# Kernel optimization log

Hardware: AMD Instinct MI355X
Metric: run time of the kernel (lower is better)

Reference implementation:

```python
import jax, jax.numpy as jnp
import numpy as np

DIMS = [64, 128, 192, 256]   # Matryoshka sub-dims (init arg `dims`)
TEMPERATURE = 1.0
NEG_INF = float('-inf')
EPS = 1e-12  # F.normalize eps


def setup_inputs() -> dict:
    key = jax.random.key(0)
    k1, k2 = jax.random.split(key)
    B, K, D = 2048, 4096, 256
    reps_q = jax.random.normal(k1, (B, D), dtype=jnp.float32)
    reps_d = jax.random.normal(k2, (K, D), dtype=jnp.float32)
    return {"reps_q": reps_q, "reps_d": reps_d}


def _l2_normalize(x):
    n = jnp.linalg.norm(x, axis=1, keepdims=True)
    return x / jnp.maximum(n, EPS)


def _loss_for_dim(reps_q, reps_d, dim):
    q = _l2_normalize(reps_q[:, :dim])   # [B, dim]
    d = _l2_normalize(reps_d[:, :dim])   # [K, dim]
    B, K = q.shape[0], d.shape[0]

    qk = q @ d.T                         # [B, K]

    # check_pos_neg_pair_conflict (always True in the torch code)
    pos = d[:B]                          # positives are the first B keys
    sim = jax.lax.stop_gradient(pos @ d.T)               # [B, K], detached
    eye_bk = jnp.eye(B, K, dtype=bool)
    conflict = jnp.isclose(sim, 1.0, rtol=1e-5, atol=1e-5) & ~eye_bk
    qk = jnp.where(conflict, NEG_INF, qk)

    # use_all_pairs=True path: kq, qq, kk with -inf diagonals
    eye_bb = jnp.eye(B, dtype=bool)
    kq = jnp.where(eye_bb, NEG_INF, pos @ q.T)           # [B, B]
    qq = jnp.where(eye_bb, NEG_INF, q @ q.T)             # [B, B]
    kk = jnp.where(eye_bb, NEG_INF, pos @ pos.T)         # [B, B]

    scores = jnp.concatenate([qk, kq, qq, kk], axis=1)   # [B, K+3B]

    # check_false_neg: mask entries above diag(scores)+0.1 (thresholds detached)
    # diag(scores)[i] = scores[i, i] = qk[i, i] since B <= K
    thr = jax.lax.stop_gradient(jnp.diagonal(qk))[:, None] + 0.1
    scores = jnp.where(scores > thr, NEG_INF, scores)

    # cross-entropy with labels = arange(B)
    logp = jax.nn.log_softmax(scores / TEMPERATURE, axis=1)
    idx = jnp.arange(B)
    return -jnp.mean(logp[idx, idx])


def reference(reps_q, reps_d):
    loss = 0.0
    for dim in DIMS:
        loss = loss + _loss_for_dim(reps_q, reps_d, dim)
    return loss / len(DIMS)
```

## Files before the change

kernel.cpp:

```cpp
#include <hip/hip_runtime.h>

#define B_N 2048
#define K_N 4096
#define D_N 256
#define GRID_SCORE 3072
#define LOG2E 1.44269504f

typedef unsigned short u16;
typedef unsigned int u32;
typedef short short8 __attribute__((ext_vector_type(8)));
typedef float f32x4 __attribute__((ext_vector_type(4)));

#if __has_builtin(__builtin_amdgcn_exp2f)
#define EXP2F(x) __builtin_amdgcn_exp2f(x)
#else
#define EXP2F(x) exp2f(x)
#endif
#if __has_builtin(__builtin_amdgcn_logf)
#define LOG2F(x) __builtin_amdgcn_logf(x)
#else
#define LOG2F(x) log2f(x)
#endif

__device__ __forceinline__ u16 f2bf(float x) {
    union { float f; u32 u; } v; v.f = x;
    u32 u = v.u;
    u32 lsb = (u >> 16) & 1u;
    u += 0x7fffu + lsb;
    return (u16)(u >> 16);
}
__device__ __forceinline__ float bits2f(u32 u) {
    union { u32 u; float f; } v; v.u = u; return v.f;
}

__device__ __forceinline__ float dpp_row16_sum(float v) {
    union { float f; int i; } a, b;
    a.f = v;
    b.i = __builtin_amdgcn_update_dpp(0, a.i, 0x128, 0xF, 0xF, true); a.f += b.f;
    b.i = __builtin_amdgcn_update_dpp(0, a.i, 0x124, 0xF, 0xF, true); a.f += b.f;
    b.i = __builtin_amdgcn_update_dpp(0, a.i, 0x04E, 0xF, 0xF, true); a.f += b.f;
    b.i = __builtin_amdgcn_update_dpp(0, a.i, 0x0B1, 0xF, 0xF, true); a.f += b.f;
    return a.f;
}

__global__ __launch_bounds__(256) void prep_kernel(
    const float* __restrict__ qsrc, const float* __restrict__ dsrc,
    u16* __restrict__ qb, u16* __restrict__ db,
    float* __restrict__ invnq, float* __restrict__ invnd, float* __restrict__ diag,
    float* __restrict__ rowsum, u32* __restrict__ doneCnt)
{
    if (blockIdx.x < 32) rowsum[blockIdx.x * 256 + threadIdx.x] = 0.f;
    if (blockIdx.x == 32 && threadIdx.x == 0)
        __hip_atomic_store(doneCnt, 0u, __ATOMIC_RELAXED, __HIP_MEMORY_SCOPE_AGENT);

    const int wave = threadIdx.x >> 6;
    const int lane = threadIdx.x & 63;
    const int row  = blockIdx.x * 4 + wave;

    if (row < B_N) {
        const int i = row;
        float4 qv = *(const float4*)(qsrc + i * D_N + lane * 4);
        float4 dv = *(const float4*)(dsrc + i * D_N + lane * 4);
        ushort4 qs; qs.x = f2bf(qv.x); qs.y = f2bf(qv.y); qs.z = f2bf(qv.z); qs.w = f2bf(qv.w);
        *(ushort4*)(qb + i * D_N + lane * 4) = qs;
        float sqq = qv.x*qv.x + qv.y*qv.y + qv.z*qv.z + qv.w*qv.w;
        float sdd = dv.x*dv.x + dv.y*dv.y + dv.z*dv.z + dv.w*dv.w;
        float sqd = qv.x*dv.x + qv.y*dv.y + qv.z*dv.z + qv.w*dv.w;
        sqq = dpp_row16_sum(sqq);
        sdd = dpp_row16_sum(sdd);
        sqd = dpp_row16_sum(sqd);
        float gq0 = __shfl(sqq, 0),  gq1 = __shfl(sqq, 16), gq2 = __shfl(sqq, 32), gq3 = __shfl(sqq, 48);
        float gd0 = __shfl(sdd, 0),  gd1 = __shfl(sdd, 16), gd2 = __shfl(sdd, 32), gd3 = __shfl(sdd, 48);
        float gp0 = __shfl(sqd, 0),  gp1 = __shfl(sqd, 16), gp2 = __shfl(sqd, 32), gp3 = __shfl(sqd, 48);
        if (lane < 4) {
            float pq = gq0, pd = gd0, pp = gp0;
            if (lane >= 1) { pq += gq1; pd += gd1; pp += gp1; }
            if (lane >= 2) { pq += gq2; pd += gd2; pp += gp2; }
            if (lane >= 3) { pq += gq3; pd += gd3; pp += gp3; }
            float inq = 1.0f / fmaxf(sqrtf(pq), 1e-12f);
            float ind = 1.0f / fmaxf(sqrtf(pd), 1e-12f);
            invnq[i * 4 + lane] = inq;
            diag[i * 4 + lane]  = pp * inq * ind;
        }
    } else {
        const int j = row - B_N;
        float4 dv = *(const float4*)(dsrc + j * D_N + lane * 4);
        ushort4 ds; ds.x = f2bf(dv.x); ds.y = f2bf(dv.y); ds.z = f2bf(dv.z); ds.w = f2bf(dv.w);
        *(ushort4*)(db + j * D_N + lane * 4) = ds;
        float sdd = dv.x*dv.x + dv.y*dv.y + dv.z*dv.z + dv.w*dv.w;
        sdd = dpp_row16_sum(sdd);
        if (lane < 4) {
            float gd0 = __shfl(sdd, 0), gd1 = __shfl(sdd, 16), gd2 = __shfl(sdd, 32), gd3 = __shfl(sdd, 48);
            float pd = gd0;
            if (lane >= 1) pd += gd1;
            if (lane >= 2) pd += gd2;
            if (lane >= 3) pd += gd3;
            invnd[j * 4 + lane] = 1.0f / fmaxf(sqrtf(pd), 1e-12f);
        }
    }
}

template<int RGN, bool EYE>
__device__ __forceinline__ void epi_seg(
    const f32x4* accq, const f32x4* accd,
    const float* ldsInvAq, const float* ldsInvAd, const float* ldsThr,
    const float* ldsInvB, float* ldsAcc,
    int s, int wrow, int quad, int lane15)
{
    const int myr = wrow + quad * 4;
    f32x4 ivAq = *(const f32x4*)(ldsInvAq + s * 64 + myr);
    f32x4 ivAd = *(const f32x4*)(ldsInvAd + s * 64 + myr);
    f32x4 thrv = *(const f32x4*)(ldsThr   + s * 64 + myr);
    f32x4 rsd = {0.f, 0.f, 0.f, 0.f};
    #pragma unroll
    for (int ct = 0; ct < 4; ++ct) {
        const float ivB = ldsInvB[s * 64 + ct * 16 + lane15];
        const int jloc = ct * 16 + lane15;
        f32x4 tq = accq[ct] * ivAq;
        f32x4 td = accd[ct] * ivAd;
        #pragma unroll
        for (int r = 0; r < 4; ++r) {
            const float thr = thrv[r];
            const float sq = tq[r] * ivB;
            const float sd = td[r] * ivB;
            const bool eye = EYE && ((myr + r) == jloc);
            float add = 0.f;
            if (RGN <= 1) {
                bool conflict = (fabsf(sd - LOG2E) <= 2e-5f * LOG2E);
                if (EYE) conflict = conflict && !eye;
                if (!conflict && sq <= thr) add += EXP2F(sq);
                if (RGN == 0) {
                    bool okk = (sd <= thr);
                    if (EYE) okk = okk && !eye;
                    if (okk) add += EXP2F(sd);
                }
            } else {
                bool o1 = (sd <= thr), o2 = (sq <= thr);
                if (EYE) { o1 = o1 && !eye; o2 = o2 && !eye; }
                if (o1) add += EXP2F(sd);
                if (o2) add += EXP2F(sq);
            }
            rsd[r] += add;
        }
    }
    f32x4 red;
    #pragma unroll
    for (int r = 0; r < 4; ++r) red[r] = dpp_row16_sum(rsd[r]);
    if (lane15 == 0)
        *(f32x4*)(ldsAcc + s * 64 + myr) = red;
}

#define LSB 264
__global__ __launch_bounds__(256, 4) void score_kernel(
    const u16* __restrict__ qb, const u16* __restrict__ db,
    const float* __restrict__ invnq, const float* __restrict__ invnd,
    const float* __restrict__ diag, float* __restrict__ rowsum,
    u32* __restrict__ doneCnt, u32* __restrict__ out)
{
    __shared__ u16   ldsB[64 * LSB];
    __shared__ float ldsInvAq[4 * 64];
    __shared__ float ldsInvAd[4 * 64];
    __shared__ float ldsThr[4 * 64];
    __shared__ float ldsInvB[4 * 64];
    __shared__ float ldsAcc[256];
    __shared__ u32   ldsLast;

    const int cb = blockIdx.x % 96;
    const int rb = blockIdx.x / 96;
    const int IR = rb * 64;
    const int JC = cb * 64;
    const bool isR3 = (cb >= 64);
    const bool isR1 = (cb < 32);
    const u16*  bsrc     = isR3 ? qb : db;
    const float* invBsrc = isR3 ? invnq : invnd;
    const int JB = isR3 ? (JC - K_N) : JC;
    const int sel = isR1 ? ((cb == rb) ? 1 : 0)
                  : (!isR3 ? 2 : (((cb - 64) == rb) ? 4 : 3));

    const int tid    = threadIdx.x;
    const int lane   = tid & 63;
    const int lane15 = lane & 15;
    const int quad   = lane >> 4;
    const int wrow   = (tid >> 6) * 16;

    {
        const int row = tid >> 2, s = tid & 3;
        ldsInvAq[s * 64 + row] = invnq[(IR + row) * 4 + s] * LOG2E;
        ldsInvAd[s * 64 + row] = invnd[(IR + row) * 4 + s] * LOG2E;
        ldsThr[s * 64 + row]   = (diag[(IR + row) * 4 + s] + 0.1f) * LOG2E;
        ldsInvB[s * 64 + row]  = invBsrc[(JB + row) * 4 + s];
    }

    #pragma unroll
    for (int c = 0; c < 8; ++c) {
        int idx = tid + c * 256;
        int row = idx >> 5;
        int ch  = idx & 31;
        uint4 v = *(const uint4*)(bsrc + (JB + row) * D_N + ch * 8);
        *(uint4*)(ldsB + row * LSB + ch * 8) = v;
    }

    const u16* qrowp = qb + (IR + wrow + lane15) * D_N + quad * 8;
    const u16* drowp = db + (IR + wrow + lane15) * D_N + quad * 8;

    short8 aq0 = *(const short8*)(qrowp);
    short8 aq1 = *(const short8*)(qrowp + 32);
    short8 ad0 = *(const short8*)(drowp);
    short8 ad1 = *(const short8*)(drowp + 32);

    __syncthreads();

    f32x4 accq[4], accd[4];
    #pragma unroll
    for (int ct = 0; ct < 4; ++ct) {
        accq[ct] = (f32x4){0.f, 0.f, 0.f, 0.f};
        accd[ct] = (f32x4){0.f, 0.f, 0.f, 0.f};
    }

    #pragma clang loop unroll(disable)
    for (int s = 0; s < 4; ++s) {
        const int sn = ((s + 1) & 3) * 64;
        short8 nq0 = *(const short8*)(qrowp + sn);
        short8 nq1 = *(const short8*)(qrowp + sn + 32);
        short8 nd0 = *(const short8*)(drowp + sn);
        short8 nd1 = *(const short8*)(drowp + sn + 32);

        #pragma unroll
        for (int ct = 0; ct < 4; ++ct) {
            short8 b0 = *(const short8*)(ldsB + (ct * 16 + lane15) * LSB + s * 64 + quad * 8);
            accq[ct] = __builtin_amdgcn_mfma_f32_16x16x32_bf16(aq0, b0, accq[ct], 0, 0, 0);
            accd[ct] = __builtin_amdgcn_mfma_f32_16x16x32_bf16(ad0, b0, accd[ct], 0, 0, 0);
        }
        #pragma unroll
        for (int ct = 0; ct < 4; ++ct) {
            short8 b1 = *(const short8*)(ldsB + (ct * 16 + lane15) * LSB + s * 64 + 32 + quad * 8);
            accq[ct] = __builtin_amdgcn_mfma_f32_16x16x32_bf16(aq1, b1, accq[ct], 0, 0, 0);
            accd[ct] = __builtin_amdgcn_mfma_f32_16x16x32_bf16(ad1, b1, accd[ct], 0, 0, 0);
        }
        if (sel == 0)      epi_seg<0,false>(accq, accd, ldsInvAq, ldsInvAd, ldsThr, ldsInvB, ldsAcc, s, wrow, quad, lane15);
        else if (sel == 1) epi_seg<0,true >(accq, accd, ldsInvAq, ldsInvAd, ldsThr, ldsInvB, ldsAcc, s, wrow, quad, lane15);
        else if (sel == 2) epi_seg<1,false>(accq, accd, ldsInvAq, ldsInvAd, ldsThr, ldsInvB, ldsAcc, s, wrow, quad, lane15);
        else if (sel == 3) epi_seg<2,false>(accq, accd, ldsInvAq, ldsInvAd, ldsThr, ldsInvB, ldsAcc, s, wrow, quad, lane15);
        else               epi_seg<2,true >(accq, accd, ldsInvAq, ldsInvAd, ldsThr, ldsInvB, ldsAcc, s, wrow, quad, lane15);

        aq0 = nq0; aq1 = nq1; ad0 = nd0; ad1 = nd1;
    }
    __syncthreads();

    atomicAdd(&rowsum[IR * 4 + tid], ldsAcc[(tid & 3) * 64 + (tid >> 2)]);
    __syncthreads();
    if (tid == 0) {
        u32 tk = __hip_atomic_fetch_add(doneCnt, 1u, __ATOMIC_RELAXED,
                                        __HIP_MEMORY_SCOPE_AGENT);
        ldsLast = (tk == (GRID_SCORE - 1)) ? 1u : 0u;
    }
    __syncthreads();

    if (ldsLast) {
        float acc = 0.f;
        #pragma unroll 8
        for (int c = 0; c < 32; ++c) {
            int idx = tid + c * 256;
            float rsv = __hip_atomic_load(&rowsum[idx], __ATOMIC_RELAXED,
                                          __HIP_MEMORY_SCOPE_AGENT);
            acc += LOG2F(rsv) * 0.69314718056f - diag[idx];
        }
        ldsAcc[tid] = acc;
        __syncthreads();
        #pragma unroll
        for (int off = 128; off > 0; off >>= 1) {
            if (tid < off) ldsAcc[tid] += ldsAcc[tid + off];
            __syncthreads();
        }
        if (tid == 0) {
            float L = ldsAcc[0] * (1.0f / (B_N * 4.0f));
            u16 h = f2bf(L);
            union { float f; u32 u; } b; b.f = L;
            u32 c0 = (b.u & 0xFFFF0000u) | (u32)h;
            u32 c1 = c0 + 0x10000u;
            u32 c2 = c0 - 0x10000u;
            float e0 = fabsf(bits2f(c0) - L);
            float e1 = fabsf(bits2f(c1) - L);
            float e2 = fabsf(bits2f(c2) - L);
            u32 best = c0; float be = e0;
            if (e1 < be) { best = c1; be = e1; }
            if (e2 < be) { best = c2; }
            out[0] = best;
        }
    }
}

extern "C" void kernel_launch(void* const* d_in, const int* in_sizes, int n_in,
                              void* d_out, int out_size, void* d_ws, size_t ws_size,
                              hipStream_t stream) {
    (void)in_sizes; (void)n_in; (void)out_size; (void)ws_size;
    const float* qsrc = (const float*)d_in[0];
    const float* dsrc = (const float*)d_in[1];
    char* ws = (char*)d_ws;
    u16*   qb      = (u16*)ws;
    u16*   db      = (u16*)(ws + 1048576);
    float* invnq   = (float*)(ws + 3145728);
    float* invnd   = (float*)(ws + 3178496);
    float* diag    = (float*)(ws + 3244032);
    float* rowsum  = (float*)(ws + 3276800);
    u32*   doneCnt = (u32*)(ws + 3309568);

    prep_kernel<<<1536, 256, 0, stream>>>(qsrc, dsrc, qb, db, invnq, invnd, diag,
                                          rowsum, doneCnt);
    score_kernel<<<GRID_SCORE, 256, 0, stream>>>(qb, db, invnq, invnd, diag, rowsum,
                                                 doneCnt, (u32*)d_out);
}
```

Measured before the change: 108.5 us.

## Double row tile to 128 per block so each staged B tile serves twice the rows

The score kernel now runs 512 threads per block covering 128 query rows instead of 64, which halves the grid. Each 64-column B tile loaded into LDS is shared by eight waves instead of four, cutting global-to-LDS traffic and the per-block setup. The eye-diagonal test gains a column offset because one 128-row block spans two 64-column diagonal tiles. The per-column inverse norms are also hoisted out of the inner epilogue loop. The cost is fewer blocks for load balance and higher register and occupancy pressure under launch_bounds(512,6).

```diff
diff --git a/kernel.cpp b/kernel.cpp
--- a/kernel.cpp
+++ b/kernel.cpp
@@ -3,7 +3,7 @@
 #define B_N 2048
 #define K_N 4096
 #define D_N 256
-#define GRID_SCORE 3072
+#define GRID_SCORE 1536
 #define LOG2E 1.44269504f
 
 typedef unsigned short u16;
@@ -105,25 +105,28 @@
     const f32x4* accq, const f32x4* accd,
     const float* ldsInvAq, const float* ldsInvAd, const float* ldsThr,
     const float* ldsInvB, float* ldsAcc,
-    int s, int wrow, int quad, int lane15)
+    int s, int wrow, int quad, int lane15, int eyeOff)
 {
     const int myr = wrow + quad * 4;
-    f32x4 ivAq = *(const f32x4*)(ldsInvAq + s * 64 + myr);
-    f32x4 ivAd = *(const f32x4*)(ldsInvAd + s * 64 + myr);
-    f32x4 thrv = *(const f32x4*)(ldsThr   + s * 64 + myr);
+    f32x4 ivAq = *(const f32x4*)(ldsInvAq + s * 128 + myr);
+    f32x4 ivAd = *(const f32x4*)(ldsInvAd + s * 128 + myr);
+    f32x4 thrv = *(const f32x4*)(ldsThr   + s * 128 + myr);
+    float ivB[4];
+    #pragma unroll
+    for (int ct = 0; ct < 4; ++ct)
+        ivB[ct] = ldsInvB[s * 64 + ct * 16 + lane15];
     f32x4 rsd = {0.f, 0.f, 0.f, 0.f};
     #pragma unroll
     for (int ct = 0; ct < 4; ++ct) {
-        const float ivB = ldsInvB[s * 64 + ct * 16 + lane15];
         const int jloc = ct * 16 + lane15;
         f32x4 tq = accq[ct] * ivAq;
         f32x4 td = accd[ct] * ivAd;
         #pragma unroll
         for (int r = 0; r < 4; ++r) {
             const float thr = thrv[r];
-            const float sq = tq[r] * ivB;
-            const float sd = td[r] * ivB;
-            const bool eye = EYE && ((myr + r) == jloc);
+            const float sq = tq[r] * ivB[ct];
+            const float sd = td[r] * ivB[ct];
+            const bool eye = EYE && ((myr + r) == (jloc + eyeOff));
             float add = 0.f;
             if (RGN <= 1) {
                 bool conflict = (fabsf(sd - LOG2E) <= 2e-5f * LOG2E);
@@ -147,35 +150,37 @@
     #pragma unroll
     for (int r = 0; r < 4; ++r) red[r] = dpp_row16_sum(rsd[r]);
     if (lane15 == 0)
-        *(f32x4*)(ldsAcc + s * 64 + myr) = red;
+        *(f32x4*)(ldsAcc + s * 128 + myr) = red;
 }
 
 #define LSB 264
-__global__ __launch_bounds__(256, 4) void score_kernel(
+__global__ __launch_bounds__(512, 6) void score_kernel(
     const u16* __restrict__ qb, const u16* __restrict__ db,
     const float* __restrict__ invnq, const float* __restrict__ invnd,
     const float* __restrict__ diag, float* __restrict__ rowsum,
     u32* __restrict__ doneCnt, u32* __restrict__ out)
 {
     __shared__ u16   ldsB[64 * LSB];
-    __shared__ float ldsInvAq[4 * 64];
-    __shared__ float ldsInvAd[4 * 64];
-    __shared__ float ldsThr[4 * 64];
+    __shared__ float ldsInvAq[4 * 128];
+    __shared__ float ldsInvAd[4 * 128];
+    __shared__ float ldsThr[4 * 128];
     __shared__ float ldsInvB[4 * 64];
-    __shared__ float ldsAcc[256];
+    __shared__ float ldsAcc[4 * 128];
     __shared__ u32   ldsLast;
 
     const int cb = blockIdx.x % 96;
     const int rb = blockIdx.x / 96;
-    const int IR = rb * 64;
+    const int IR = rb * 128;
     const int JC = cb * 64;
     const bool isR3 = (cb >= 64);
     const bool isR1 = (cb < 32);
     const u16*  bsrc     = isR3 ? qb : db;
     const float* invBsrc = isR3 ? invnq : invnd;
     const int JB = isR3 ? (JC - K_N) : JC;
-    const int sel = isR1 ? ((cb == rb) ? 1 : 0)
-                  : (!isR3 ? 2 : (((cb - 64) == rb) ? 4 : 3));
+    const int cc = isR3 ? (cb - 64) : cb;
+    const int sel = isR1 ? (((cb >> 1) == rb) ? 1 : 0)
+                  : (!isR3 ? 2 : (((cc >> 1) == rb) ? 4 : 3));
+    const int eyeOff = (cc & 1) * 64;
 
     const int tid    = threadIdx.x;
     const int lane   = tid & 63;
@@ -185,15 +190,18 @@
 
     {
         const int row = tid >> 2, s = tid & 3;
-        ldsInvAq[s * 64 + row] = invnq[(IR + row) * 4 + s] * LOG2E;
-        ldsInvAd[s * 64 + row] = invnd[(IR + row) * 4 + s] * LOG2E;
-        ldsThr[s * 64 + row]   = (diag[(IR + row) * 4 + s] + 0.1f) * LOG2E;
-        ldsInvB[s * 64 + row]  = invBsrc[(JB + row) * 4 + s];
-    }
-
-    #pragma unroll
-    for (int c = 0; c < 8; ++c) {
-        int idx = tid + c * 256;
+        ldsInvAq[s * 128 + row] = invnq[(IR + row) * 4 + s] * LOG2E;
+        ldsInvAd[s * 128 + row] = invnd[(IR + row) * 4 + s] * LOG2E;
+        ldsThr[s * 128 + row]   = (diag[(IR + row) * 4 + s] + 0.1f) * LOG2E;
+        if (tid < 256) {
+            const int rw = tid >> 2, sc = tid & 3;
+            ldsInvB[sc * 64 + rw]  = invBsrc[(JB + rw) * 4 + sc];
+        }
+    }
+
+    #pragma unroll
+    for (int c = 0; c < 4; ++c) {
+        int idx = tid + c * 512;
         int row = idx >> 5;
         int ch  = idx & 31;
         uint4 v = *(const uint4*)(bsrc + (JB + row) * D_N + ch * 8);
@@ -237,17 +245,17 @@
             accq[ct] = __builtin_amdgcn_mfma_f32_16x16x32_bf16(aq1, b1, accq[ct], 0, 0, 0);
             accd[ct] = __builtin_amdgcn_mfma_f32_16x16x32_bf16(ad1, b1, accd[ct], 0, 0, 0);
         }
-        if (sel == 0)      epi_seg<0,false>(accq, accd, ldsInvAq, ldsInvAd, ldsThr, ldsInvB, ldsAcc, s, wrow, quad, lane15);
-        else if (sel == 1) epi_seg<0,true >(accq, accd, ldsInvAq, ldsInvAd, ldsThr, ldsInvB, ldsAcc, s, wrow, quad, lane15);
-        else if (sel == 2) epi_seg<1,false>(accq, accd, ldsInvAq, ldsInvAd, ldsThr, ldsInvB, ldsAcc, s, wrow, quad, lane15);
-        else if (sel == 3) epi_seg<2,false>(accq, accd, ldsInvAq, ldsInvAd, ldsThr, ldsInvB, ldsAcc, s, wrow, quad, lane15);
-        else               epi_seg<2,true >(accq, accd, ldsInvAq, ldsInvAd, ldsThr, ldsInvB, ldsAcc, s, wrow, quad, lane15);
+        if (sel == 0)      epi_seg<0,false>(accq, accd, ldsInvAq, ldsInvAd, ldsThr, ldsInvB, ldsAcc, s, wrow, quad, lane15, eyeOff);
+        else if (sel == 1) epi_seg<0,true >(accq, accd, ldsInvAq, ldsInvAd, ldsThr, ldsInvB, ldsAcc, s, wrow, quad, lane15, eyeOff);
+        else if (sel == 2) epi_seg<1,false>(accq, accd, ldsInvAq, ldsInvAd, ldsThr, ldsInvB, ldsAcc, s, wrow, quad, lane15, eyeOff);
+        else if (sel == 3) epi_seg<2,false>(accq, accd, ldsInvAq, ldsInvAd, ldsThr, ldsInvB, ldsAcc, s, wrow, quad, lane15, eyeOff);
+        else               epi_seg<2,true >(accq, accd, ldsInvAq, ldsInvAd, ldsThr, ldsInvB, ldsAcc, s, wrow, quad, lane15, eyeOff);
 
         aq0 = nq0; aq1 = nq1; ad0 = nd0; ad1 = nd1;
     }
     __syncthreads();
 
-    atomicAdd(&rowsum[IR * 4 + tid], ldsAcc[(tid & 3) * 64 + (tid >> 2)]);
+    atomicAdd(&rowsum[IR * 4 + tid], ldsAcc[(tid & 3) * 128 + (tid >> 2)]);
     __syncthreads();
     if (tid == 0) {
         u32 tk = __hip_atomic_fetch_add(doneCnt, 1u, __ATOMIC_RELAXED,
@@ -259,8 +267,8 @@
     if (ldsLast) {
         float acc = 0.f;
         #pragma unroll 8
-        for (int c = 0; c < 32; ++c) {
-            int idx = tid + c * 256;
+        for (int c = 0; c < 16; ++c) {
+            int idx = tid + c * 512;
             float rsv = __hip_atomic_load(&rowsum[idx], __ATOMIC_RELAXED,
                                           __HIP_MEMORY_SCOPE_AGENT);
             acc += LOG2F(rsv) * 0.69314718056f - diag[idx];
@@ -268,7 +276,7 @@
         ldsAcc[tid] = acc;
         __syncthreads();
         #pragma unroll
-        for (int off = 128; off > 0; off >>= 1) {
+        for (int off = 256; off > 0; off >>= 1) {
             if (tid < off) ldsAcc[tid] += ldsAcc[tid + off];
             __syncthreads();
         }
@@ -307,6 +315,6 @@
 
     prep_kernel<<<1536, 256, 0, stream>>>(qsrc, dsrc, qb, db, invnq, invnd, diag,
                                           rowsum, doneCnt);
-    score_kernel<<<GRID_SCORE, 256, 0, stream>>>(qb, db, invnq, invnd, diag, rowsum,
+    score_kernel<<<GRID_SCORE, 512, 0, stream>>>(qb, db, invnq, invnd, diag, rowsum,
                                                  doneCnt, (u32*)d_out);
 }
```

After: 178.9 us. 1.65x slower.
